# Kernel tuning notes

Hardware: AMD Instinct MI355X
Metric: run time of the kernel (lower is better)

## Reference

```python
import jax, jax.numpy as jnp
import numpy as np

B, HW, NTGT, C = 2, 4096, 4096, 512
H, KNN = 8, 32
DH = C // H
SCALE = DH ** -0.5


def setup_inputs() -> dict:
    key = jax.random.key(0)
    ks = jax.random.split(key, 12)
    s = 1.0 / np.sqrt(C)
    return {
        "src": jax.random.normal(ks[0], (B, HW, C), jnp.float32),
        "tgt": jax.random.normal(ks[1], (B, NTGT, C), jnp.float32),
        "indices": jax.random.randint(ks[2], (B, HW, KNN), 0, NTGT, jnp.int64),
        "weights": jax.random.normal(ks[3], (B, HW, KNN), jnp.float32),
        "Wq": jax.random.normal(ks[4], (C, C), jnp.float32) * s,
        "bq": jnp.zeros((C,), jnp.float32),
        "Wk": jax.random.normal(ks[5], (C, C), jnp.float32) * s,
        "bk": jnp.zeros((C,), jnp.float32),
        "Wv": jax.random.normal(ks[6], (C, C), jnp.float32) * s,
        "bv": jnp.zeros((C,), jnp.float32),
        "Wo": jax.random.normal(ks[7], (C, C), jnp.float32) * s,
        "bo": jnp.zeros((C,), jnp.float32),
    }


def reference(src, tgt, indices, weights, Wq, bq, Wk, bk, Wv, bv, Wo, bo):
    b, hw, c = src.shape
    # projections -> (b, H, seq, dh)
    q = (src @ Wq + bq).reshape(b, hw, H, DH).transpose(0, 2, 1, 3)
    k = (tgt @ Wk + bk).reshape(b, -1, H, DH).transpose(0, 2, 1, 3)
    v = (tgt @ Wv + bv).reshape(b, -1, H, DH).transpose(0, 2, 1, 3)
    # gather epipolar neighbors: per batch, kb[:, idx] -> (H, hw, KNN, dh)
    gather = jax.vmap(lambda xb, ib: xb[:, ib])
    k_g = gather(k, indices)  # (b, H, hw, KNN, dh)
    v_g = gather(v, indices)  # (b, H, hw, KNN, dh)
    logits = jnp.einsum("bhqd,bhqkd->bhqk", q, k_g) * SCALE
    logits = logits + weights[:, None]  # broadcast over heads
    attn = jax.nn.softmax(logits, axis=-1)
    out = jnp.einsum("bhqk,bhqkd->bhqd", attn, v_g)
    out = out.transpose(0, 2, 1, 3).reshape(b, hw, c)
    return out @ Wo + bo
```

## Files before the change

kernel.cpp:

```cpp
#include <hip/hip_runtime.h>
#include <hip/hip_bf16.h>
#include <stdint.h>
#include <type_traits>

#define B_    2
#define HW_   4096
#define NTGT_ 4096
#define C_    512
#define H_    8
#define KNN_  32
#define DH_   64
#define M_    (B_ * HW_)

typedef unsigned short ushort_t;
typedef _Float16 f16x8 __attribute__((ext_vector_type(8)));
typedef __fp16 hf2 __attribute__((ext_vector_type(2)));
typedef float floatx4 __attribute__((ext_vector_type(4)));

__device__ __forceinline__ uint32_t pkh(float x, float y) {
    union { hf2 h; uint32_t u; } c;
    c.h = __builtin_amdgcn_cvt_pkrtz(x, y);
    return c.u;
}
__device__ __forceinline__ ushort_t f2h(float f) {
    return (ushort_t)(pkh(f, 0.f) & 0xffffu);
}
__device__ __forceinline__ float h2f(ushort_t u) {
    union { ushort_t s; __fp16 h; } x;
    x.s = u;
    return (float)x.h;
}
__device__ __forceinline__ ushort_t f2b(float f) {
    union { float f; uint32_t i; } x;
    x.f = f;
    uint32_t r = x.i + 0x7fffu + ((x.i >> 16) & 1u);
    return (ushort_t)(r >> 16);
}
__device__ __forceinline__ float dot2acc(uint32_t a, uint32_t b, float c) {
#if __has_builtin(__builtin_amdgcn_fdot2)
    union { uint32_t u; hf2 h; } xa, xb;
    xa.u = a; xb.u = b;
    return __builtin_amdgcn_fdot2(xa.h, xb.h, c, false);
#else
    c = fmaf(h2f((ushort_t)(a & 0xffffu)), h2f((ushort_t)(b & 0xffffu)), c);
    return fmaf(h2f((ushort_t)(a >> 16)), h2f((ushort_t)(b >> 16)), c);
#endif
}
__device__ __forceinline__ uint4 pack8(const float4& a, const float4& b) {
    return make_uint4(pkh(a.x, a.y), pkh(a.z, a.w), pkh(b.x, b.y), pkh(b.z, b.w));
}

__global__ __launch_bounds__(256) void transpose_cvt4(
    const float* __restrict__ W0, const float* __restrict__ W1,
    const float* __restrict__ W2, const float* __restrict__ W3,
    ushort_t* __restrict__ T0, ushort_t* __restrict__ T1,
    ushort_t* __restrict__ T2, ushort_t* __restrict__ T3) {
    __shared__ float tile[32][33];

    const float* W = (blockIdx.z == 0) ? W0 : (blockIdx.z == 1) ? W1
                     : (blockIdx.z == 2) ? W2 : W3;
    ushort_t* T = (blockIdx.z == 0) ? T0 : (blockIdx.z == 1) ? T1
                  : (blockIdx.z == 2) ? T2 : T3;

    const int k0 = blockIdx.x * 32;
    const int n0 = blockIdx.y * 32;
    const int t = threadIdx.x;
    const int r = t >> 3;
    const int c0 = (t & 7) * 4;

    float4 d = *(const float4*)&W[(size_t)(k0 + r) * 512 + n0 + c0];
    tile[r][c0 + 0] = d.x; tile[r][c0 + 1] = d.y;
    tile[r][c0 + 2] = d.z; tile[r][c0 + 3] = d.w;
    __syncthreads();

    uint2 o;
    o.x = pkh(tile[c0 + 0][r], tile[c0 + 1][r]);
    o.y = pkh(tile[c0 + 2][r], tile[c0 + 3][r]);
    *(uint2*)&T[(size_t)(n0 + r) * 512 + k0 + c0] = o;
}

__global__ __launch_bounds__(256) void transpose_inplace4_f32(
    float* W0, float* W1, float* W2, float* W3) {
    __shared__ float ta[32][33];
    __shared__ float tb[32][33];

    float* W = (blockIdx.y == 0) ? W0 : (blockIdx.y == 1) ? W1
               : (blockIdx.y == 2) ? W2 : W3;

    int p = blockIdx.x;
    int i = 0, acc = 0;
    while (acc + (16 - i) <= p) { acc += 16 - i; ++i; }
    const int j = i + (p - acc);

    const int t = threadIdx.x;
    const int r = t >> 3;
    const int c0 = (t & 7) * 4;

    {
        float4 d = *(const float4*)&W[(size_t)(i * 32 + r) * 512 + j * 32 + c0];
        ta[r][c0 + 0] = d.x; ta[r][c0 + 1] = d.y;
        ta[r][c0 + 2] = d.z; ta[r][c0 + 3] = d.w;
    }
    if (i != j) {
        float4 d = *(const float4*)&W[(size_t)(j * 32 + r) * 512 + i * 32 + c0];
        tb[r][c0 + 0] = d.x; tb[r][c0 + 1] = d.y;
        tb[r][c0 + 2] = d.z; tb[r][c0 + 3] = d.w;
    }
    __syncthreads();

    *(float4*)&W[(size_t)(j * 32 + r) * 512 + i * 32 + c0] =
        make_float4(ta[c0 + 0][r], ta[c0 + 1][r], ta[c0 + 2][r], ta[c0 + 3][r]);
    if (i != j)
        *(float4*)&W[(size_t)(i * 32 + r) * 512 + j * 32 + c0] =
            make_float4(tb[c0 + 0][r], tb[c0 + 1][r], tb[c0 + 2][r], tb[c0 + 3][r]);
}

template <typename AT, typename BT, typename OT, int BN, bool OBF16>
__device__ __forceinline__ void gemm_body(const AT* __restrict__ A,
                                          const BT* __restrict__ Wt,
                                          const float* __restrict__ bias,
                                          OT* __restrict__ O,
                                          int bm, int bn) {
    constexpr int NJ = BN / 32;
    __shared__ ushort_t As[128][40];
    __shared__ ushort_t Bs[BN][40];

    const int t = threadIdx.x;
    const int lr = t >> 2;
    const int lc = (t & 3) * 8;

    const int lane = t & 63;
    const int wv = t >> 6;
    const int wr = (wv >> 1) * 64;
    const int wc = (wv & 1) * (BN / 2);
    const int r16 = lane & 15;
    const int quad = lane >> 4;

    floatx4 acc[4][NJ] = {};

    float4 fa0, fa1, fa2, fa3, fb0, fb1, fb2, fb3;
    uint4 ua0, ua1, ub0, ub1;

    if constexpr (std::is_same<AT, float>::value) {
        const float* p0 = &A[(size_t)(bm + lr) * 512 + lc];
        const float* p1 = &A[(size_t)(bm + lr + 64) * 512 + lc];
        fa0 = *(const float4*)p0; fa1 = *(const float4*)(p0 + 4);
        fa2 = *(const float4*)p1; fa3 = *(const float4*)(p1 + 4);
    } else {
        ua0 = *(const uint4*)&A[(size_t)(bm + lr) * 512 + lc];
        ua1 = *(const uint4*)&A[(size_t)(bm + lr + 64) * 512 + lc];
    }
    if constexpr (std::is_same<BT, float>::value) {
        const float* p0 = &Wt[(size_t)(bn + lr) * 512 + lc];
        fb0 = *(const float4*)p0; fb1 = *(const float4*)(p0 + 4);
        if constexpr (BN == 128) {
            const float* p1 = &Wt[(size_t)(bn + lr + 64) * 512 + lc];
            fb2 = *(const float4*)p1; fb3 = *(const float4*)(p1 + 4);
        }
    } else {
        ub0 = *(const uint4*)&Wt[(size_t)(bn + lr) * 512 + lc];
        if constexpr (BN == 128)
            ub1 = *(const uint4*)&Wt[(size_t)(bn + lr + 64) * 512 + lc];
    }

    for (int kt = 0; kt < 512; kt += 32) {
        __syncthreads();
        if constexpr (std::is_same<AT, float>::value) {
            *(uint4*)&As[lr][lc] = pack8(fa0, fa1);
            *(uint4*)&As[lr + 64][lc] = pack8(fa2, fa3);
        } else {
            *(uint4*)&As[lr][lc] = ua0;
            *(uint4*)&As[lr + 64][lc] = ua1;
        }
        if constexpr (std::is_same<BT, float>::value) {
            *(uint4*)&Bs[lr][lc] = pack8(fb0, fb1);
            if constexpr (BN == 128) *(uint4*)&Bs[lr + 64][lc] = pack8(fb2, fb3);
        } else {
            *(uint4*)&Bs[lr][lc] = ub0;
            if constexpr (BN == 128) *(uint4*)&Bs[lr + 64][lc] = ub1;
        }
        __syncthreads();

        if (kt + 32 < 512) {
            const int k2 = kt + 32;
            if constexpr (std::is_same<AT, float>::value) {
                const float* p0 = &A[(size_t)(bm + lr) * 512 + k2 + lc];
                const float* p1 = &A[(size_t)(bm + lr + 64) * 512 + k2 + lc];
                fa0 = *(const float4*)p0; fa1 = *(const float4*)(p0 + 4);
                fa2 = *(const float4*)p1; fa3 = *(const float4*)(p1 + 4);
            } else {
                ua0 = *(const uint4*)&A[(size_t)(bm + lr) * 512 + k2 + lc];
                ua1 = *(const uint4*)&A[(size_t)(bm + lr + 64) * 512 + k2 + lc];
            }
            if constexpr (std::is_same<BT, float>::value) {
                const float* p0 = &Wt[(size_t)(bn + lr) * 512 + k2 + lc];
                fb0 = *(const float4*)p0; fb1 = *(const float4*)(p0 + 4);
                if constexpr (BN == 128) {
                    const float* p1 = &Wt[(size_t)(bn + lr + 64) * 512 + k2 + lc];
                    fb2 = *(const float4*)p1; fb3 = *(const float4*)(p1 + 4);
                }
            } else {
                ub0 = *(const uint4*)&Wt[(size_t)(bn + lr) * 512 + k2 + lc];
                if constexpr (BN == 128)
                    ub1 = *(const uint4*)&Wt[(size_t)(bn + lr + 64) * 512 + k2 + lc];
            }
        }

        f16x8 af[4], bf[NJ];
#pragma unroll
        for (int i = 0; i < 4; ++i)
            af[i] = *(const f16x8*)&As[wr + i * 16 + r16][quad * 8];
#pragma unroll
        for (int j = 0; j < NJ; ++j)
            bf[j] = *(const f16x8*)&Bs[wc + j * 16 + r16][quad * 8];
#pragma unroll
        for (int i = 0; i < 4; ++i)
#pragma unroll
            for (int j = 0; j < NJ; ++j)
                acc[i][j] = __builtin_amdgcn_mfma_f32_16x16x32_f16(
                    af[i], bf[j], acc[i][j], 0, 0, 0);
    }

#pragma unroll
    for (int j = 0; j < NJ; ++j) {
        const int col = bn + wc + j * 16 + r16;
        const float bj = bias[col];
#pragma unroll
        for (int i = 0; i < 4; ++i) {
            const int row = bm + wr + i * 16 + quad * 4;
#pragma unroll
            for (int r = 0; r < 4; ++r) {
                float v = acc[i][j][r] + bj;
                if constexpr (std::is_same<OT, float>::value)
                    O[(size_t)(row + r) * 512 + col] = v;
                else if constexpr (OBF16)
                    O[(size_t)(row + r) * 512 + col] = f2b(v);
                else
                    O[(size_t)(row + r) * 512 + col] = f2h(v);
            }
        }
    }
}

template <typename BT>
__global__ __launch_bounds__(256, 3) void gemm_qkv(
    const float* __restrict__ src, const float* __restrict__ tgt,
    const BT* __restrict__ WtQ, const BT* __restrict__ WtK,
    const BT* __restrict__ WtV,
    const float* __restrict__ bq, const float* __restrict__ bk,
    const float* __restrict__ bv,
    ushort_t* __restrict__ Qb, ushort_t* __restrict__ Kb,
    ushort_t* __restrict__ Vb) {
    const int id = blockIdx.x;
    const int xcd = id & 7;
    const int g = id >> 3;
    const int mgrp = g / 12;
    const int r = g % 12;
    const int z = r >> 2;
    const int bn = (r & 3) * 128;
    const int bm = (xcd + 8 * mgrp) * 128;

    const float* A = (z == 0) ? src : tgt;
    const BT* Wt = (z == 0) ? WtQ : (z == 1) ? WtK : WtV;
    const float* bias = (z == 0) ? bq : (z == 1) ? bk : bv;
    ushort_t* O = (z == 0) ? Qb : (z == 1) ? Kb : Vb;
    gemm_body<float, BT, ushort_t, 128, false>(A, Wt, bias, O, bm, bn);
}

template <typename BT, typename OT, bool OBF16>
__global__ __launch_bounds__(256, 4) void gemm_o(const ushort_t* __restrict__ A,
                                                 const BT* __restrict__ Wt,
                                                 const float* __restrict__ bias,
                                                 OT* __restrict__ O) {
    const int id = blockIdx.x;
    const int xcd = id & 7;
    const int g = id >> 3;
    const int mgrp = g >> 3;
    const int bn = (g & 7) * 64;
    const int bm = (xcd + 8 * mgrp) * 128;
    gemm_body<ushort_t, BT, OT, 64, OBF16>(A, Wt, bias, O, bm, bn);
}

#define KVSTRIDE 520
template <typename IT>
__global__ __launch_bounds__(256, 7) void attn_kernel(const ushort_t* Q,
                                                      const ushort_t* __restrict__ K,
                                                      const ushort_t* __restrict__ V,
                                                      const IT* __restrict__ idx,
                                                      const float* __restrict__ wts,
                                                      ushort_t* O) {
    __shared__ uint32_t qs[16][20];
    __shared__ ushort_t kvs[16][KVSTRIDE];
    __shared__ float ps[H_][KNN_];
    __shared__ int idxs[KNN_];
    __shared__ float ws[KNN_];

    const int t = threadIdx.x;
    const int id = blockIdx.x;
    const int xcd = id & 7;
    const int slot = id >> 3;
    const int b = xcd >> 2;
    const int bq = b * HW_ + (xcd & 3) * 1024 + slot;
    const size_t qoff = (size_t)bq * C_;

    qs[t >> 4][t & 15] = *(const uint32_t*)(Q + qoff + 2 * t);
    if (t < KNN_) {
        idxs[t] = (int)idx[(size_t)bq * KNN_ + t];
        ws[t] = wts[(size_t)bq * KNN_ + t];
    }
    __syncthreads();

    const ushort_t* Kbase = K + (size_t)b * NTGT_ * C_;
    const ushort_t* Vbase = V + (size_t)b * NTGT_ * C_;
    const int prow = t >> 4;
    const int pcol = (t & 15) * 8;

    const int h = t >> 5;
    const int l5 = t & 31;
    const int nl = l5 & 15;
    const int half = l5 >> 4;
    const int koff = h * 64 + half * 32;

    uint4 r0, r1, r2, r3;
    {
        const ushort_t* p = Kbase + (size_t)idxs[prow] * C_ + pcol;
        r0 = *(const uint4*)(p);       r1 = *(const uint4*)(p + 128);
        r2 = *(const uint4*)(p + 256); r3 = *(const uint4*)(p + 384);
    }
    const int qrow = h * 2 + half;
    uint4 q0 = *(const uint4*)&qs[qrow][0];
    uint4 q1 = *(const uint4*)&qs[qrow][4];
    uint4 q2 = *(const uint4*)&qs[qrow][8];
    uint4 q3 = *(const uint4*)&qs[qrow][12];

    *(uint4*)&kvs[prow][pcol + 0]   = r0;
    *(uint4*)&kvs[prow][pcol + 128] = r1;
    *(uint4*)&kvs[prow][pcol + 256] = r2;
    *(uint4*)&kvs[prow][pcol + 384] = r3;
    {
        const ushort_t* p = Kbase + (size_t)idxs[prow + 16] * C_ + pcol;
        r0 = *(const uint4*)(p);       r1 = *(const uint4*)(p + 128);
        r2 = *(const uint4*)(p + 256); r3 = *(const uint4*)(p + 384);
    }
    __syncthreads();

    float l0, l1;
    {
        uint4 kv0 = *(const uint4*)&kvs[nl][koff + 0];
        uint4 kv1 = *(const uint4*)&kvs[nl][koff + 8];
        uint4 kv2 = *(const uint4*)&kvs[nl][koff + 16];
        uint4 kv3 = *(const uint4*)&kvs[nl][koff + 24];
        float da = 0.f, db = 0.f;
        da = dot2acc(kv0.x, q0.x, da); da = dot2acc(kv0.y, q0.y, da);
        da = dot2acc(kv0.z, q0.z, da); da = dot2acc(kv0.w, q0.w, da);
        db = dot2acc(kv1.x, q1.x, db); db = dot2acc(kv1.y, q1.y, db);
        db = dot2acc(kv1.z, q1.z, db); db = dot2acc(kv1.w, q1.w, db);
        da = dot2acc(kv2.x, q2.x, da); da = dot2acc(kv2.y, q2.y, da);
        da = dot2acc(kv2.z, q2.z, da); da = dot2acc(kv2.w, q2.w, da);
        db = dot2acc(kv3.x, q3.x, db); db = dot2acc(kv3.y, q3.y, db);
        db = dot2acc(kv3.z, q3.z, db); db = dot2acc(kv3.w, q3.w, db);
        float dot = da + db;
        dot += __shfl_xor(dot, 16);
        l0 = dot * 0.125f + ws[nl];
    }
    __syncthreads();
    *(uint4*)&kvs[prow][pcol + 0]   = r0;
    *(uint4*)&kvs[prow][pcol + 128] = r1;
    *(uint4*)&kvs[prow][pcol + 256] = r2;
    *(uint4*)&kvs[prow][pcol + 384] = r3;
    {
        const ushort_t* p = Vbase + (size_t)idxs[prow] * C_ + pcol;
        r0 = *(const uint4*)(p);       r1 = *(const uint4*)(p + 128);
        r2 = *(const uint4*)(p + 256); r3 = *(const uint4*)(p + 384);
    }
    __syncthreads();
    {
        uint4 kv0 = *(const uint4*)&kvs[nl][koff + 0];
        uint4 kv1 = *(const uint4*)&kvs[nl][koff + 8];
        uint4 kv2 = *(const uint4*)&kvs[nl][koff + 16];
        uint4 kv3 = *(const uint4*)&kvs[nl][koff + 24];
        float da = 0.f, db = 0.f;
        da = dot2acc(kv0.x, q0.x, da); da = dot2acc(kv0.y, q0.y, da);
        da = dot2acc(kv0.z, q0.z, da); da = dot2acc(kv0.w, q0.w, da);
        db = dot2acc(kv1.x, q1.x, db); db = dot2acc(kv1.y, q1.y, db);
        db = dot2acc(kv1.z, q1.z, db); db = dot2acc(kv1.w, q1.w, db);
        da = dot2acc(kv2.x, q2.x, da); da = dot2acc(kv2.y, q2.y, da);
        da = dot2acc(kv2.z, q2.z, da); da = dot2acc(kv2.w, q2.w, da);
        db = dot2acc(kv3.x, q3.x, db); db = dot2acc(kv3.y, q3.y, db);
        db = dot2acc(kv3.z, q3.z, db); db = dot2acc(kv3.w, q3.w, db);
        float dot = da + db;
        dot += __shfl_xor(dot, 16);
        l1 = dot * 0.125f + ws[nl + 16];
    }
    {
        float m = fmaxf(l0, l1);
#pragma unroll
        for (int o = 16; o > 0; o >>= 1) m = fmaxf(m, __shfl_xor(m, o));
        float e0 = __expf(l0 - m), e1 = __expf(l1 - m);
        float s = e0 + e1;
#pragma unroll
        for (int o = 16; o > 0; o >>= 1) s += __shfl_xor(s, o);
        const float inv = 2.0f / s;
        ps[h][nl] = e0 * inv;
        ps[h][nl + 16] = e1 * inv;
    }
    __syncthreads();
    *(uint4*)&kvs[prow][pcol + 0]   = r0;
    *(uint4*)&kvs[prow][pcol + 128] = r1;
    *(uint4*)&kvs[prow][pcol + 256] = r2;
    *(uint4*)&kvs[prow][pcol + 384] = r3;
    {
        const ushort_t* p = Vbase + (size_t)idxs[prow + 16] * C_ + pcol;
        r0 = *(const uint4*)(p);       r1 = *(const uint4*)(p + 128);
        r2 = *(const uint4*)(p + 256); r3 = *(const uint4*)(p + 384);
    }
    __syncthreads();

    const int d2 = l5 * 2;
    float a0 = 0.f, a1 = 0.f;
#pragma unroll
    for (int nn = 0; nn < 16; ++nn) {
        uint32_t vv = *(const uint32_t*)&kvs[nn][h * DH_ + d2];
        float p = ps[h][nn];
        a0 = fmaf(p, h2f((ushort_t)(vv & 0xffffu)), a0);
        a1 = fmaf(p, h2f((ushort_t)(vv >> 16)), a1);
    }
    __syncthreads();
    *(uint4*)&kvs[prow][pcol + 0]   = r0;
    *(uint4*)&kvs[prow][pcol + 128] = r1;
    *(uint4*)&kvs[prow][pcol + 256] = r2;
    *(uint4*)&kvs[prow][pcol + 384] = r3;
    __syncthreads();
#pragma unroll
    for (int nn = 0; nn < 16; ++nn) {
        uint32_t vv = *(const uint32_t*)&kvs[nn][h * DH_ + d2];
        float p = ps[h][nn + 16];
        a0 = fmaf(p, h2f((ushort_t)(vv & 0xffffu)), a0);
        a1 = fmaf(p, h2f((ushort_t)(vv >> 16)), a1);
    }
    *(uint32_t*)(O + qoff + h * DH_ + d2) = pkh(a0, a1);
}

static int elem_bytes(const void* p, size_t n, int dflt) {
    size_t sz = 0;
    hipError_t err = hipPointerGetAttribute(
        &sz, HIP_POINTER_ATTRIBUTE_RANGE_SIZE, (hipDeviceptr_t)(uintptr_t)p);
    if (err == hipSuccess && sz >= n && (sz % n) == 0) {
        size_t b = sz / n;
        if (b == 2 || b == 4 || b == 8) return (int)b;
    }
    return dflt;
}

extern "C" void kernel_launch(void* const* d_in, const int* in_sizes, int n_in,
                              void* d_out, int out_size, void* d_ws, size_t ws_size,
                              hipStream_t stream) {
    const float* src  = (const float*)d_in[0];
    const float* tgt  = (const float*)d_in[1];
    const void*  idxp = d_in[2];
    const float* wtp  = (const float*)d_in[3];
    float* Wq = (float*)d_in[4];  const float* bq = (const float*)d_in[5];
    float* Wk = (float*)d_in[6];  const float* bk = (const float*)d_in[7];
    float* Wv = (float*)d_in[8];  const float* bv = (const float*)d_in[9];
    float* Wo = (float*)d_in[10]; const float* bo = (const float*)d_in[11];

    const size_t NELEM = (size_t)M_ * C_;
    const size_t WELEM = (size_t)C_ * C_;
    const size_t NIDX  = (size_t)B_ * HW_ * KNN_;

    const int ib = elem_bytes(idxp, NIDX, 4);
    const int ob = elem_bytes(d_out, NELEM, 4);

    dim3 blk(256);

    ushort_t* Qb = (ushort_t*)d_ws;
    ushort_t* Kb = Qb + NELEM;
    ushort_t* Vb = (ushort_t*)d_out;
    ushort_t* Ob = Qb;

    const bool wfit = ws_size >= (2 * NELEM + 4 * WELEM) * sizeof(ushort_t);

    if (wfit) {
        ushort_t* T = Kb + NELEM;
        ushort_t* WtQ = T;
        ushort_t* WtK = T + WELEM;
        ushort_t* WtV = T + 2 * WELEM;
        ushort_t* WtO = T + 3 * WELEM;

        transpose_cvt4<<<dim3(16, 16, 4), blk, 0, stream>>>(
            Wq, Wk, Wv, Wo, WtQ, WtK, WtV, WtO);

        gemm_qkv<ushort_t><<<dim3(768), blk, 0, stream>>>(
            src, tgt, WtQ, WtK, WtV, bq, bk, bv, Qb, Kb, Vb);

        if (ib == 8)
            attn_kernel<long long><<<dim3(B_ * HW_), blk, 0, stream>>>(
                Qb, Kb, Vb, (const long long*)idxp, wtp, Ob);
        else
            attn_kernel<int><<<dim3(B_ * HW_), blk, 0, stream>>>(
                Qb, Kb, Vb, (const int*)idxp, wtp, Ob);

        if (ob == 2)
            gemm_o<ushort_t, ushort_t, true><<<dim3(512), blk, 0, stream>>>(
                Ob, WtO, bo, (ushort_t*)d_out);
        else
            gemm_o<ushort_t, float, false><<<dim3(512), blk, 0, stream>>>(
                Ob, WtO, bo, (float*)d_out);
    } else {
        transpose_inplace4_f32<<<dim3(136, 4), blk, 0, stream>>>(Wq, Wk, Wv, Wo);

        gemm_qkv<float><<<dim3(768), blk, 0, stream>>>(
            src, tgt, Wq, Wk, Wv, bq, bk, bv, Qb, Kb, Vb);

        if (ib == 8)
            attn_kernel<long long><<<dim3(B_ * HW_), blk, 0, stream>>>(
                Qb, Kb, Vb, (const long long*)idxp, wtp, Ob);
        else
            attn_kernel<int><<<dim3(B_ * HW_), blk, 0, stream>>>(
                Qb, Kb, Vb, (const int*)idxp, wtp, Ob);

        if (ob == 2)
            gemm_o<float, ushort_t, true><<<dim3(512), blk, 0, stream>>>(
                Ob, Wo, bo, (ushort_t*)d_out);
        else
            gemm_o<float, float, false><<<dim3(512), blk, 0, stream>>>(
                Ob, Wo, bo, (float*)d_out);
    }
}
```

Before: 181.9 us.

## Issue all K/V gather loads up front and drop shared-memory staging of Q/idx/weights

The attention kernel now reads indices, weights and Q directly from global memory into registers instead of staging them through shared memory behind a barrier. It also issues the loads for all four 16-row K/V tiles early, keeping three in flight at once, rather than prefetching one tile at a time. The aim is to expose more memory-level parallelism for the random row gathers and remove one barrier. The cost is many more live registers, so launch bounds drop from 7 to 5 blocks per SIMD, which lowers occupancy.

```diff
diff --git a/kernel.cpp b/kernel.cpp
--- a/kernel.cpp
+++ b/kernel.cpp
@@ -283,64 +283,67 @@
 
 #define KVSTRIDE 520
 template <typename IT>
-__global__ __launch_bounds__(256, 7) void attn_kernel(const ushort_t* Q,
-                                                      const ushort_t* __restrict__ K,
-                                                      const ushort_t* __restrict__ V,
-                                                      const IT* __restrict__ idx,
-                                                      const float* __restrict__ wts,
-                                                      ushort_t* O) {
-    __shared__ uint32_t qs[16][20];
+__global__ __launch_bounds__(256, 5) void attn_kernel(
+    const ushort_t* __restrict__ Q, const ushort_t* __restrict__ K,
+    const ushort_t* __restrict__ V, const IT* __restrict__ idx,
+    const float* __restrict__ wts, ushort_t* O) {
     __shared__ ushort_t kvs[16][KVSTRIDE];
     __shared__ float ps[H_][KNN_];
-    __shared__ int idxs[KNN_];
-    __shared__ float ws[KNN_];
 
     const int t = threadIdx.x;
     const int id = blockIdx.x;
     const int xcd = id & 7;
     const int slot = id >> 3;
-    const int b = xcd >> 2;
-    const int bq = b * HW_ + (xcd & 3) * 1024 + slot;
+    const int bt = xcd >> 2;
+    const int bq = bt * HW_ + (xcd & 3) * 1024 + slot;
     const size_t qoff = (size_t)bq * C_;
-
-    qs[t >> 4][t & 15] = *(const uint32_t*)(Q + qoff + 2 * t);
-    if (t < KNN_) {
-        idxs[t] = (int)idx[(size_t)bq * KNN_ + t];
-        ws[t] = wts[(size_t)bq * KNN_ + t];
-    }
-    __syncthreads();
-
-    const ushort_t* Kbase = K + (size_t)b * NTGT_ * C_;
-    const ushort_t* Vbase = V + (size_t)b * NTGT_ * C_;
-    const int prow = t >> 4;
-    const int pcol = (t & 15) * 8;
 
     const int h = t >> 5;
     const int l5 = t & 31;
     const int nl = l5 & 15;
     const int half = l5 >> 4;
     const int koff = h * 64 + half * 32;
-
-    uint4 r0, r1, r2, r3;
-    {
-        const ushort_t* p = Kbase + (size_t)idxs[prow] * C_ + pcol;
-        r0 = *(const uint4*)(p);       r1 = *(const uint4*)(p + 128);
-        r2 = *(const uint4*)(p + 256); r3 = *(const uint4*)(p + 384);
-    }
-    const int qrow = h * 2 + half;
-    uint4 q0 = *(const uint4*)&qs[qrow][0];
-    uint4 q1 = *(const uint4*)&qs[qrow][4];
-    uint4 q2 = *(const uint4*)&qs[qrow][8];
-    uint4 q3 = *(const uint4*)&qs[qrow][12];
-
-    *(uint4*)&kvs[prow][pcol + 0]   = r0;
-    *(uint4*)&kvs[prow][pcol + 128] = r1;
-    *(uint4*)&kvs[prow][pcol + 256] = r2;
-    *(uint4*)&kvs[prow][pcol + 384] = r3;
-    {
-        const ushort_t* p = Kbase + (size_t)idxs[prow + 16] * C_ + pcol;
-        r0 = *(const uint4*)(p);       r1 = *(const uint4*)(p + 128);
-        r2 = *(const uint4*)(p + 256); r3 = *(const uint4*)(p + 384);
+    const int prow = t >> 4;
+    const int pcol = (t & 15) * 8;
+
+    const IT* ibp = idx + (size_t)bq * KNN_;
+    const int i0 = (int)ibp[prow];
+    const int i1 = (int)ibp[prow + 16];
+    const float w0 = wts[(size_t)bq * KNN_ + nl];
+    const float w1 = wts[(size_t)bq * KNN_ + nl + 16];
+    const ushort_t* qp = Q + qoff + koff;
+    const uint4 q0 = *(const uint4*)(qp);
+    const uint4 q1 = *(const uint4*)(qp + 8);
+    const uint4 q2 = *(const uint4*)(qp + 16);
+    const uint4 q3 = *(const uint4*)(qp + 24);
+
+    const ushort_t* Kbase = K + (size_t)bt * NTGT_ * C_;
+    const ushort_t* Vbase = V + (size_t)bt * NTGT_ * C_;
+
+    uint4 a0, a1, a2, a3, b0, b1, b2, b3, c0, c1, c2, c3;
+    {
+        const ushort_t* p = Kbase + (size_t)i0 * C_ + pcol;
+        a0 = *(const uint4*)(p);       a1 = *(const uint4*)(p + 128);
+        a2 = *(const uint4*)(p + 256); a3 = *(const uint4*)(p + 384);
+    }
+    {
+        const ushort_t* p = Kbase + (size_t)i1 * C_ + pcol;
+        b0 = *(const uint4*)(p);       b1 = *(const uint4*)(p + 128);
+        b2 = *(const uint4*)(p + 256); b3 = *(const uint4*)(p + 384);
+    }
+    {
+        const ushort_t* p = Vbase + (size_t)i0 * C_ + pcol;
+        c0 = *(const uint4*)(p);       c1 = *(const uint4*)(p + 128);
+        c2 = *(const uint4*)(p + 256); c3 = *(const uint4*)(p + 384);
+    }
+    *(uint4*)&kvs[prow][pcol + 0]   = a0;
+    *(uint4*)&kvs[prow][pcol + 128] = a1;
+    *(uint4*)&kvs[prow][pcol + 256] = a2;
+    *(uint4*)&kvs[prow][pcol + 384] = a3;
+    {
+        const ushort_t* p = Vbase + (size_t)i1 * C_ + pcol;
+        a0 = *(const uint4*)(p);       a1 = *(const uint4*)(p + 128);
+        a2 = *(const uint4*)(p + 256); a3 = *(const uint4*)(p + 384);
     }
     __syncthreads();
 
@@ -361,18 +364,13 @@
         db = dot2acc(kv3.z, q3.z, db); db = dot2acc(kv3.w, q3.w, db);
         float dot = da + db;
         dot += __shfl_xor(dot, 16);
-        l0 = dot * 0.125f + ws[nl];
-    }
-    __syncthreads();
-    *(uint4*)&kvs[prow][pcol + 0]   = r0;
-    *(uint4*)&kvs[prow][pcol + 128] = r1;
-    *(uint4*)&kvs[prow][pcol + 256] = r2;
-    *(uint4*)&kvs[prow][pcol + 384] = r3;
-    {
-        const ushort_t* p = Vbase + (size_t)idxs[prow] * C_ + pcol;
-        r0 = *(const uint4*)(p);       r1 = *(const uint4*)(p + 128);
-        r2 = *(const uint4*)(p + 256); r3 = *(const uint4*)(p + 384);
-    }
+        l0 = dot * 0.125f + w0;
+    }
+    __syncthreads();
+    *(uint4*)&kvs[prow][pcol + 0]   = b0;
+    *(uint4*)&kvs[prow][pcol + 128] = b1;
+    *(uint4*)&kvs[prow][pcol + 256] = b2;
+    *(uint4*)&kvs[prow][pcol + 384] = b3;
     __syncthreads();
     {
         uint4 kv0 = *(const uint4*)&kvs[nl][koff + 0];
@@ -390,7 +388,7 @@
         db = dot2acc(kv3.z, q3.z, db); db = dot2acc(kv3.w, q3.w, db);
         float dot = da + db;
         dot += __shfl_xor(dot, 16);
-        l1 = dot * 0.125f + ws[nl + 16];
+        l1 = dot * 0.125f + w1;
     }
     {
         float m = fmaxf(l0, l1);
@@ -405,40 +403,35 @@
         ps[h][nl + 16] = e1 * inv;
     }
     __syncthreads();
-    *(uint4*)&kvs[prow][pcol + 0]   = r0;
-    *(uint4*)&kvs[prow][pcol + 128] = r1;
-    *(uint4*)&kvs[prow][pcol + 256] = r2;
-    *(uint4*)&kvs[prow][pcol + 384] = r3;
-    {
-        const ushort_t* p = Vbase + (size_t)idxs[prow + 16] * C_ + pcol;
-        r0 = *(const uint4*)(p);       r1 = *(const uint4*)(p + 128);
-        r2 = *(const uint4*)(p + 256); r3 = *(const uint4*)(p + 384);
-    }
+    *(uint4*)&kvs[prow][pcol + 0]   = c0;
+    *(uint4*)&kvs[prow][pcol + 128] = c1;
+    *(uint4*)&kvs[prow][pcol + 256] = c2;
+    *(uint4*)&kvs[prow][pcol + 384] = c3;
     __syncthreads();
 
     const int d2 = l5 * 2;
-    float a0 = 0.f, a1 = 0.f;
+    float f0 = 0.f, f1 = 0.f;
 #pragma unroll
     for (int nn = 0; nn < 16; ++nn) {
         uint32_t vv = *(const uint32_t*)&kvs[nn][h * DH_ + d2];
         float p = ps[h][nn];
-        a0 = fmaf(p, h2f((ushort_t)(vv & 0xffffu)), a0);
-        a1 = fmaf(p, h2f((ushort_t)(vv >> 16)), a1);
-    }
-    __syncthreads();
-    *(uint4*)&kvs[prow][pcol + 0]   = r0;
-    *(uint4*)&kvs[prow][pcol + 128] = r1;
-    *(uint4*)&kvs[prow][pcol + 256] = r2;
-    *(uint4*)&kvs[prow][pcol + 384] = r3;
+        f0 = fmaf(p, h2f((ushort_t)(vv & 0xffffu)), f0);
+        f1 = fmaf(p, h2f((ushort_t)(vv >> 16)), f1);
+    }
+    __syncthreads();
+    *(uint4*)&kvs[prow][pcol + 0]   = a0;
+    *(uint4*)&kvs[prow][pcol + 128] = a1;
+    *(uint4*)&kvs[prow][pcol + 256] = a2;
+    *(uint4*)&kvs[prow][pcol + 384] = a3;
     __syncthreads();
 #pragma unroll
     for (int nn = 0; nn < 16; ++nn) {
         uint32_t vv = *(const uint32_t*)&kvs[nn][h * DH_ + d2];
         float p = ps[h][nn + 16];
-        a0 = fmaf(p, h2f((ushort_t)(vv & 0xffffu)), a0);
-        a1 = fmaf(p, h2f((ushort_t)(vv >> 16)), a1);
-    }
-    *(uint32_t*)(O + qoff + h * DH_ + d2) = pkh(a0, a1);
+        f0 = fmaf(p, h2f((ushort_t)(vv & 0xffffu)), f0);
+        f1 = fmaf(p, h2f((ushort_t)(vv >> 16)), f1);
+    }
+    *(uint32_t*)(O + qoff + h * DH_ + d2) = pkh(f0, f1);
 }
 
 static int elem_bytes(const void* p, size_t n, int dflt) {
```

Measured after the change: 178.0 us. 2.2% less time.
